# Kernel optimization log

Measured on AMD Instinct MI355X. Metric: run time of the kernel, lower is better.

## Reference

```python
import jax, jax.numpy as jnp
import numpy as np

N, E, H, HEADS, L, B = 16000, 256000, 192, 4, 4, 8
C = H // HEADS
VN, VE, T = 32, 8, 1000


def _sin_emb(t, dim):
    half = dim // 2
    freqs = jnp.exp(-np.log(10000.0) * jnp.arange(half, dtype=jnp.float32) / half)
    ang = t.astype(jnp.float32)[:, None] * freqs[None, :]
    return jnp.concatenate([jnp.sin(ang), jnp.cos(ang)], axis=-1)


def _ln(x, g, b, eps=1e-5):
    mu = jnp.mean(x, -1, keepdims=True)
    var = jnp.mean(jnp.square(x - mu), -1, keepdims=True)
    return (x - mu) * jax.lax.rsqrt(var + eps) * g + b


def setup_inputs():
    key = jax.random.key(0)
    ks = iter(jax.random.split(key, 64))
    p = lambda shape, s=0.02: jax.random.normal(next(ks), shape, jnp.float32) * s
    inp = {}
    inp['node_emb'] = p((VN, H))
    inp['edge_emb'] = p((VE, H))
    inp['time_w1'] = p((H, H)); inp['time_b1'] = jnp.zeros((H,), jnp.float32)
    inp['time_w2'] = p((H, H)); inp['time_b2'] = jnp.zeros((H,), jnp.float32)
    inp['mask_emb'] = p((2, H))
    inp['wq'] = p((L, H, H)); inp['bq'] = jnp.zeros((L, H), jnp.float32)
    inp['wk'] = p((L, H, H)); inp['bk'] = jnp.zeros((L, H), jnp.float32)
    inp['wv'] = p((L, H, H)); inp['bv'] = jnp.zeros((L, H), jnp.float32)
    inp['we'] = p((L, H, H))
    inp['wskip'] = p((L, H, H)); inp['bskip'] = jnp.zeros((L, H), jnp.float32)
    inp['wbeta'] = p((L, 3 * H))
    inp['ln_g'] = jnp.ones((L, H), jnp.float32); inp['ln_b'] = jnp.zeros((L, H), jnp.float32)
    inp['node_out_w'] = p((H, VN)); inp['node_out_b'] = jnp.zeros((VN,), jnp.float32)
    inp['edge_w1'] = p((4 * H, H)); inp['edge_b1'] = jnp.zeros((H,), jnp.float32)
    inp['edge_w2'] = p((H, VE)); inp['edge_b2'] = jnp.zeros((VE,), jnp.float32)
    inp['node_type'] = jax.random.randint(next(ks), (N,), 0, VN)
    inp['edge_type'] = jax.random.randint(next(ks), (E,), 0, VE)
    inp['edge_index'] = jax.random.randint(next(ks), (2, E), 0, N)
    inp['edit_mask'] = jax.random.randint(next(ks), (N,), 0, 2, dtype=jnp.int32)
    inp['node_batch'] = jnp.sort(jax.random.randint(next(ks), (N,), 0, B))
    inp['t_graph'] = jax.random.randint(next(ks), (B,), 1, T)
    return inp


def reference(node_emb, edge_emb, time_w1, time_b1, time_w2, time_b2, mask_emb,
              wq, bq, wk, bk, wv, bv, we, wskip, bskip, wbeta, ln_g, ln_b,
              node_out_w, node_out_b, edge_w1, edge_b1, edge_w2, edge_b2,
              node_type, edge_type, edge_index, edit_mask, node_batch, t_graph):
    src, dst = edge_index[0], edge_index[1]
    # time embedding: sinusoidal -> Linear -> SiLU -> Linear  => [B, H]
    t_vec = jax.nn.silu(_sin_emb(t_graph, H) @ time_w1 + time_b1) @ time_w2 + time_b2
    t_node = t_vec[node_batch]              # [N, H]
    t_edge = t_vec[node_batch[src]]         # [E, H]
    x = node_emb[node_type] + t_node + mask_emb[edit_mask]
    edge_attr = edge_emb[edge_type] + t_edge
    scale = 1.0 / np.sqrt(C)
    for l in range(L):
        q = (x @ wq[l] + bq[l]).reshape(N, HEADS, C)
        k = (x @ wk[l] + bk[l]).reshape(N, HEADS, C)
        v = (x @ wv[l] + bv[l]).reshape(N, HEADS, C)
        e = (edge_attr @ we[l]).reshape(E, HEADS, C)
        kj = k[src] + e                                   # [E, heads, C]
        score = jnp.sum(q[dst] * kj, axis=-1) * scale      # [E, heads]
        m = jax.ops.segment_max(score, dst, num_segments=N)
        ex = jnp.exp(score - m[dst])
        denom = jax.ops.segment_sum(ex, dst, num_segments=N)
        alpha = ex / denom[dst]
        msg = (v[src] + e) * alpha[..., None]              # [E, heads, C]
        out = jax.ops.segment_sum(msg, dst, num_segments=N).reshape(N, H)
        xr = x @ wskip[l] + bskip[l]
        beta = jax.nn.sigmoid(jnp.concatenate([out, xr, out - xr], -1) @ wbeta[l])[:, None]
        h = beta * xr + (1.0 - beta) * out
        x = _ln(x + h, ln_g[l], ln_b[l])
    node_logits = x @ node_out_w + node_out_b
    edge_feat = jnp.concatenate([x[src], x[dst], edge_attr, t_edge], -1)  # [E, 4H]
    edge_logits = jax.nn.silu(edge_feat @ edge_w1 + edge_b1) @ edge_w2 + edge_b2
    return node_logits, edge_logits
```

## Files before the change

kernel.cpp:

```cpp
#include <hip/hip_runtime.h>
#include <hip/hip_bf16.h>
#include <math.h>

#define NN 16000
#define NPAD 16128
#define NE 256000
#define H 192
#define RP 256
#define KVR 512
#define NL 4
#define NBATCH 8
#define VEt 8
#define HH (H*H)
#define EML 16

typedef __hip_bfloat16 bf16;
typedef unsigned short u16;
typedef unsigned char u8;
typedef unsigned int u32;
typedef __attribute__((ext_vector_type(8))) short bfrag_t;
typedef __attribute__((ext_vector_type(4))) float facc_t;
typedef __attribute__((ext_vector_type(4))) float f4;
typedef __attribute__((ext_vector_type(2))) unsigned int u32x2;
typedef __attribute__((ext_vector_type(2))) float f2v;

__device__ __forceinline__ bf16 f2b(float v){ return __float2bfloat16(v); }
__device__ __forceinline__ int rfl(int v){ return __builtin_amdgcn_readfirstlane(v); }

__device__ __forceinline__ unsigned enc8sw(float x){
    unsigned u = __float_as_uint(x);
    unsigned s = (u >> 24) & 0x80u;
    float ax = fabsf(x);
    if(ax >= 448.f) return s | 0x7Eu;
    if(ax < 0.015625f){
        int q = (int)rintf(ax * 512.f);
        return s | (unsigned)q;
    }
    unsigned au = u & 0x7FFFFFFFu;
    unsigned lsb = (au >> 20) & 1u;
    au += 0x7FFFFu + lsb;
    unsigned E = (au >> 23) - 127u;
    unsigned M = (au >> 20) & 7u;
    if((int)E > 8) return s | 0x7Eu;
    return s | ((E + 7u) << 3) | M;
}
__device__ __forceinline__ unsigned enc8(float x){
#if __has_builtin(__builtin_amdgcn_cvt_pk_fp8_f32)
    return (u32)__builtin_amdgcn_cvt_pk_fp8_f32(x, x, 0, false) & 0xFFu;
#else
    return enc8sw(x);
#endif
}
template<int SEL>
__device__ __forceinline__ float dec8s(u32 w){
#if __has_builtin(__builtin_amdgcn_cvt_f32_fp8)
    return __builtin_amdgcn_cvt_f32_fp8((int)w, SEL);
#else
    unsigned v = (w >> (SEL*8)) & 0xFFu;
    unsigned e = (v >> 3) & 15u, m = v & 7u;
    float mag = e ? __builtin_ldexpf((float)(8u + m), (int)e - 10)
                  : __builtin_ldexpf((float)m, -9);
    return (v & 0x80u) ? -mag : mag;
#endif
}
__device__ __forceinline__ f2v dec8pk01(u32 w){
#if __has_builtin(__builtin_amdgcn_cvt_pk_f32_fp8)
    return __builtin_amdgcn_cvt_pk_f32_fp8((int)w, false);
#else
    f2v r; r.x = dec8s<0>(w); r.y = dec8s<1>(w); return r;
#endif
}
__device__ __forceinline__ float frcp(float x){
#if __has_builtin(__builtin_amdgcn_rcpf)
    return __builtin_amdgcn_rcpf(x);
#else
    return 1.f/x;
#endif
}

__global__ void k_sentinel(float* __restrict__ out, float v){ out[0] = v; }

__global__ void k_prep0(const float* __restrict__ wq, const float* __restrict__ wk,
                        const float* __restrict__ wv, const float* __restrict__ wsk,
                        const float* __restrict__ w1, const float* __restrict__ now,
                        const float* __restrict__ ew2, u16* __restrict__ wt,
                        const int* __restrict__ tg, const float* __restrict__ tw1,
                        const float* __restrict__ tb1, const float* __restrict__ tw2,
                        const float* __restrict__ tb2, float* __restrict__ tvec,
                        int* __restrict__ cnt){
    int blk = blockIdx.x;
    if(blk < 160){
        int mat = blk >> 3, ys = blk & 7;
        if(mat < 18){
            const float* src;
            if(mat < 4)       src = wq  + (size_t)mat*HH;
            else if(mat < 8)  src = wk  + (size_t)(mat-4)*HH;
            else if(mat < 12) src = wv  + (size_t)(mat-8)*HH;
            else if(mat < 16) src = wsk + (size_t)(mat-12)*HH;
            else              src = w1  + (size_t)(mat-16)*HH;
            u16* dst = wt + (size_t)mat*HH;
            const int slice = HH/8;
            int base = ys*slice;
            for(int i = base + threadIdx.x; i < base + slice; i += blockDim.x){
                int k = i / H, n = i % H;
                bf16 b = f2b(src[i]);
                dst[n*H + k] = *(u16*)&b;
            }
        } else if(mat == 18){
            u16* dst = wt + (size_t)18*HH;
            const int slice = (32*192)/8;
            int base = ys*slice;
            for(int i = base + threadIdx.x; i < base + slice; i += blockDim.x){
                int k = i >> 5, n = i & 31;
                bf16 b = f2b(now[i]);
                dst[n*192 + k] = *(u16*)&b;
            }
        } else {
            u16* dst = wt + (size_t)18*HH + 32*192;
            const int slice = (16*192)/8;
            int base = ys*slice;
            for(int i = base + threadIdx.x; i < base + slice; i += blockDim.x){
                int k = i >> 4, n = i & 15;
                float v = (n < 8) ? ew2[k*8 + n] : 0.f;
                bf16 b = f2b(v);
                dst[n*192 + k] = *(u16*)&b;
            }
        }
    } else if(blk < 168){
        int b = blk - 160, j = threadIdx.x;
        __shared__ float emb[H], h1[H];
        float t = (float)tg[b];
        if(j < 96){
            float fr = __expf(-logf(10000.0f) * (float)j / 96.0f);
            float ang = t * fr;
            emb[j]      = sinf(ang);
            emb[j + 96] = cosf(ang);
        }
        __syncthreads();
        if(j < H){
            float acc = tb1[j];
            for(int k = 0; k < H; k++) acc += emb[k] * tw1[k*H + j];
            h1[j] = acc / (1.f + __expf(-acc));
        }
        __syncthreads();
        if(j < H){
            float acc2 = tb2[j];
            for(int k = 0; k < H; k++) acc2 += h1[k] * tw2[k*H + j];
            tvec[b*H + j] = acc2;
        }
    } else {
        int i = (blk - 168)*256 + threadIdx.x;
        if(i < NN+1) cnt[i] = 0;
    }
}

__global__ void k_prep1(const float* __restrict__ nemb, const float* __restrict__ memb,
                        const float* __restrict__ tvec, const int* __restrict__ ntype,
                        const int* __restrict__ emask, const int* __restrict__ nbatch,
                        float* __restrict__ x, u16* __restrict__ xb,
                        const int* __restrict__ edst, int* __restrict__ cnt,
                        const float* __restrict__ eemb, const float* __restrict__ we,
                        const float* __restrict__ w1, const float* __restrict__ b1,
                        u16* __restrict__ etab, u16* __restrict__ ctab){
    int blk = blockIdx.x;
    if(blk < 3000){
        int idx4 = (blk*256 + threadIdx.x)*4;
        int n = idx4 / H, c = idx4 % H;
        f4 nv = *(const f4*)(nemb + (size_t)ntype[n]*H + c);
        f4 tv = *(const f4*)(tvec + (size_t)nbatch[n]*H + c);
        f4 mv = *(const f4*)(memb + (size_t)emask[n]*H + c);
        f4 v; v.x = nv.x+tv.x+mv.x; v.y = nv.y+tv.y+mv.y;
              v.z = nv.z+tv.z+mv.z; v.w = nv.w+tv.w+mv.w;
        *(f4*)(x + idx4) = v;
        bf16 b0 = f2b(v.x), b1v = f2b(v.y), b2 = f2b(v.z), b3 = f2b(v.w);
        u16* xbp = xb + idx4;
        xbp[0] = *(u16*)&b0; xbp[1] = *(u16*)&b1v; xbp[2] = *(u16*)&b2; xbp[3] = *(u16*)&b3;
    } else if(blk < 4000){
        int e = (blk - 3000)*256 + threadIdx.x;
        atomicAdd(&cnt[edst[e]], 1);
    } else {
        int blk2 = blk - 4000;
        int c = threadIdx.x;
        __shared__ float a[H];
        if(blk2 < NL*64){
            int l = blk2 >> 6, idx = blk2 & 63, b = idx >> 3, et = idx & 7;
            if(c < H) a[c] = eemb[et*H + c] + tvec[b*H + c];
            __syncthreads();
            if(c < H){
                float acc = 0.f;
                const float* w = we + (size_t)l*HH;
                for(int k = 0; k < H; k++) acc += a[k] * w[k*H + c];
                bf16 bv = f2b(acc);
                etab[(size_t)blk2*256 + (c/3)*4 + (c%3)] = *(u16*)&bv;
            }
        } else {
            int idx = blk2 - NL*64, b = idx >> 3, et = idx & 7;
            if(c < H) a[c] = eemb[et*H + c] + tvec[b*H + c];
            __syncthreads();
            if(c < H){
                float acc = b1[c];
                for(int k = 0; k < H; k++){
                    acc += a[k]          * w1[(size_t)(2*H + k)*H + c];
                    acc += tvec[b*H + k] * w1[(size_t)(3*H + k)*H + c];
                }
                bf16 bv = f2b(acc);
                ctab[(size_t)idx*256 + (c/3)*4 + (c%3)] = *(u16*)&bv;
            }
        }
    }
}

__global__ __launch_bounds__(1024) void k_scan(const int* __restrict__ cnt,
                                               int* __restrict__ ofs, int* __restrict__ cur){
    __shared__ int wsum[16];
    __shared__ int carry_s;
    int tid = threadIdx.x, lane = tid & 63, w = tid >> 6;
    if(tid == 0) carry_s = 0;
    __syncthreads();
    for(int base = 0; base < NN; base += 1024){
        int idx = base + tid;
        int v = (idx < NN) ? cnt[idx] : 0;
        int sc = v;
        #pragma unroll
        for(int o = 1; o < 64; o <<= 1){
            int t = __shfl_up(sc, o);
            if(lane >= o) sc += t;
        }
        if(lane == 63) wsum[w] = sc;
        __syncthreads();
        if(w == 0){
            int ws = (lane < 16) ? wsum[lane] : 0;
            #pragma unroll
            for(int o = 1; o < 16; o <<= 1){
                int t = __shfl_up(ws, o);
                if(lane >= o) ws += t;
            }
            if(lane < 16) wsum[lane] = ws;
        }
        __syncthreads();
        int wbase = (w > 0) ? wsum[w-1] : 0;
        int c = carry_s;
        int excl = c + wbase + sc - v;
        if(idx < NN){ ofs[idx] = excl; cur[idx] = excl; }
        __syncthreads();
        if(tid == 0) carry_s = c + wsum[15];
        __syncthreads();
    }
    if(threadIdx.x == 0) ofs[NN] = carry_s;
}
__global__ void k_scatter(const int* __restrict__ esrc, const int* __restrict__ edst,
                          const int* __restrict__ etype, const int* __restrict__ nbatch,
                          int* __restrict__ cur, int2* __restrict__ spair, int4* __restrict__ eprep){
    int e = blockIdx.x*blockDim.x + threadIdx.x;
    if(e >= NE) return;
    int s = esrc[e], d = edst[e];
    int ct = (nbatch[s]*VEt + etype[e])*KVR;
    int pos = atomicAdd(&cur[d], 1);
    int2 se; se.x = s*KVR; se.y = ct;
    spair[pos] = se;
    eprep[e] = make_int4(s*RP, d*RP, ct, 0);
}

struct GemmP {
    const u16* wt[4];
    const float* bias[4];
    void* out[4];
    int obf[4];
};
__global__ __launch_bounds__(256) void k_gemm(const u16* __restrict__ A, GemmP P){
    int oi = blockIdx.y / 3, nt = blockIdx.y % 3;
    const u16* Wt = P.wt[oi];
    const float* bias = P.bias[oi];
    int wave = rfl(threadIdx.x >> 6), lane = threadIdx.x & 63;
    int quad = lane >> 4, l16 = lane & 15;
    int m0 = blockIdx.x*256 + wave*64;
    int n0 = nt*64;
    facc_t acc[4][4];
    #pragma unroll
    for(int i = 0; i < 4; i++)
        #pragma unroll
        for(int j = 0; j < 4; j++){ acc[i][j][0]=0.f; acc[i][j][1]=0.f; acc[i][j][2]=0.f; acc[i][j][3]=0.f; }
    #pragma unroll
    for(int kc = 0; kc < 6; kc++){
        int kb = kc*32 + quad*8;
        bfrag_t af[4], bg[4];
        #pragma unroll
        for(int i = 0; i < 4; i++) af[i] = *(const bfrag_t*)(A  + (size_t)(m0 + i*16 + l16)*H + kb);
        #pragma unroll
        for(int j = 0; j < 4; j++) bg[j] = *(const bfrag_t*)(Wt + (size_t)(n0 + j*16 + l16)*H + kb);
        #pragma unroll
        for(int i = 0; i < 4; i++)
            #pragma unroll
            for(int j = 0; j < 4; j++)
                acc[i][j] = __builtin_amdgcn_mfma_f32_16x16x32_bf16(af[i], bg[j], acc[i][j], 0, 0, 0);
    }
    float bv[4];
    #pragma unroll
    for(int j = 0; j < 4; j++) bv[j] = bias ? bias[n0 + j*16 + l16] : 0.f;
    int mode = P.obf[oi];
    if(mode == 5){
        u16* outp = (u16*)P.out[oi];
        int hoff[4];
        #pragma unroll
        for(int j = 0; j < 4; j++){
            int c = n0 + j*16 + l16;
            hoff[j] = (c/3)*4 + (c%3);
        }
        #pragma unroll
        for(int i = 0; i < 4; i++){
            int rb = m0 + i*16 + quad*4;
            #pragma unroll
            for(int r = 0; r < 4; r++){
                int row = rb + r;
                if(row < NN){
                    #pragma unroll
                    for(int j = 0; j < 4; j++){
                        bf16 b = f2b(acc[i][j][r] + bv[j]);
                        outp[(size_t)row*256 + hoff[j]] = *(u16*)&b;
                    }
                }
            }
        }
    } else if(mode != 0){
        u8* out = (u8*)P.out[oi];
        int rstride = (mode == 2) ? RP : KVR;
        int mult    = (mode == 2) ? 4  : 8;
        int koff    = (mode == 4) ? 4  : 0;
        int byteoff[4];
        #pragma unroll
        for(int j = 0; j < 4; j++){
            int c = n0 + j*16 + l16;
            byteoff[j] = (c/3)*mult + (c%3) + koff;
        }
        #pragma unroll
        for(int i = 0; i < 4; i++){
            int rb = m0 + i*16 + quad*4;
            #pragma unroll
            for(int r = 0; r < 4; r++){
                int row = rb + r;
                if(row < NN){
                    #pragma unroll
                    for(int j = 0; j < 4; j++)
                        out[(size_t)row*rstride + byteoff[j]] = (u8)enc8(acc[i][j][r] + bv[j]);
                }
            }
        }
    } else {
        float* out = (float*)P.out[oi];
        #pragma unroll
        for(int i = 0; i < 4; i++){
            int rb = m0 + i*16 + quad*4;
            #pragma unroll
            for(int r = 0; r < 4; r++){
                int row = rb + r;
                if(row < NN){
                    #pragma unroll
                    for(int j = 0; j < 4; j++)
                        out[(size_t)row*H + n0 + j*16 + l16] = acc[i][j][r] + bv[j];
                }
            }
        }
    }
}

__global__ __launch_bounds__(256) void k_attn(
    const u8* __restrict__ Qb, const u8* __restrict__ KVb,
    const u8* __restrict__ XRp,
    const u16* __restrict__ etab, const int* __restrict__ ofs,
    const int2* __restrict__ spair,
    const float* __restrict__ wb, const float* __restrict__ lng, const float* __restrict__ lnb,
    float* __restrict__ x, u16* __restrict__ xb)
{
    int wv = rfl(threadIdx.x >> 6);
    int n = blockIdx.x*4 + wv;
    int lane = threadIdx.x & 63;
    int lane8 = lane*8;
    int ch = lane*3;
    size_t base = (size_t)n*H + ch;
    const float scale = 0.14433756729740646f;
    u32x2 qw = *(const u32x2*)(Qb + (size_t)n*512 + lane8);
    float q0 = __uint_as_float(qw.x << 16);
    float q1 = __uint_as_float(qw.x & 0xffff0000u);
    float q2 = __uint_as_float(qw.y << 16);
    int p0 = ofs[n], p1 = ofs[n+1];
    float lac[4]  = {0.f,0.f,0.f,0.f};
    float ac0[4]  = {0.f,0.f,0.f,0.f};
    float ac1[4]  = {0.f,0.f,0.f,0.f};
    float ac2[4]  = {0.f,0.f,0.f,0.f};
    const u8* etb = (const u8*)etab;
    int p = p0;
    u32x2 kvc[4], ewc[4];
    bool have = (p + 3 < p1);
    if(have){
        #pragma unroll
        for(int t = 0; t < 4; t++){
            int2 se = spair[p+t];
            kvc[t] = *(const u32x2*)(KVb + se.x + lane8);
            ewc[t] = *(const u32x2*)(etb + se.y + lane8);
        }
    }
    while(have){
        int pn = p + 4;
        bool more = (pn + 3 < p1);
        u32x2 kvn[4], ewn[4];
        if(more){
            #pragma unroll
            for(int t = 0; t < 4; t++){
                int2 se = spair[pn+t];
                kvn[t] = *(const u32x2*)(KVb + se.x + lane8);
                ewn[t] = *(const u32x2*)(etb + se.y + lane8);
            }
        }
        float e0[4], e1[4], e2[4], tt[4];
        #pragma unroll
        for(int t = 0; t < 4; t++){
            e0[t] = __uint_as_float(ewc[t].x << 16);
            e1[t] = __uint_as_float(ewc[t].x & 0xffff0000u);
            e2[t] = __uint_as_float(ewc[t].y << 16);
            f2v k01 = dec8pk01(kvc[t].x);
            float k2 = dec8s<2>(kvc[t].x);
            tt[t] = q0*(k01.x+e0[t]) + q1*(k01.y+e1[t]) + q2*(k2+e2[t]);
        }
        #pragma unroll
        for(int o = 1; o <= 8; o <<= 1){
            #pragma unroll
            for(int t = 0; t < 4; t++) tt[t] += __shfl_xor(tt[t], o);
        }
        #pragma unroll
        for(int t = 0; t < 4; t++){
            float sc = fminf(fmaxf(tt[t]*scale, -60.f), 60.f);
            float pw = __expf(sc);
            f2v v01 = dec8pk01(kvc[t].y);
            float v2 = dec8s<2>(kvc[t].y);
            lac[t] += pw;
            ac0[t] += pw*(v01.x+e0[t]);
            ac1[t] += pw*(v01.y+e1[t]);
            ac2[t] += pw*(v2+e2[t]);
        }
        if(more){
            #pragma unroll
            for(int t = 0; t < 4; t++){ kvc[t] = kvn[t]; ewc[t] = ewn[t]; }
        }
        p = pn;
        have = more;
    }
    for(; p < p1; p++){
        int soA = spair[p].x, eoA = spair[p].y;
        u32x2 kvA = *(const u32x2*)(KVb + soA + lane8);
        u32x2 ewA = *(const u32x2*)(etb + eoA + lane8);
        float e0A = __uint_as_float(ewA.x << 16);
        float e1A = __uint_as_float(ewA.x & 0xffff0000u);
        float e2A = __uint_as_float(ewA.y << 16);
        f2v k01 = dec8pk01(kvA.x);
        float k2 = dec8s<2>(kvA.x);
        float tA = q0*(k01.x+e0A) + q1*(k01.y+e1A) + q2*(k2+e2A);
        tA += __shfl_xor(tA,1); tA += __shfl_xor(tA,2); tA += __shfl_xor(tA,4); tA += __shfl_xor(tA,8);
        float sc = fminf(fmaxf(tA*scale, -60.f), 60.f);
        float pw = __expf(sc);
        f2v v01 = dec8pk01(kvA.y);
        float v2 = dec8s<2>(kvA.y);
        lac[0] += pw;
        ac0[0] += pw*(v01.x+e0A);
        ac1[0] += pw*(v01.y+e1A);
        ac2[0] += pw*(v2+e2A);
    }
    float l  = (lac[0]+lac[1]) + (lac[2]+lac[3]);
    float a0 = (ac0[0]+ac0[1]) + (ac0[2]+ac0[3]);
    float a1 = (ac1[0]+ac1[1]) + (ac1[2]+ac1[3]);
    float a2 = (ac2[0]+ac2[1]) + (ac2[2]+ac2[3]);
    float inv = (p1 > p0) ? 1.f/l : 0.f;
    float o0 = a0*inv, o1 = a1*inv, o2 = a2*inv;
    u32x2 xrw = *(const u32x2*)(XRp + (size_t)n*512 + lane8);
    float xr0 = __uint_as_float(xrw.x << 16);
    float xr1 = __uint_as_float(xrw.x & 0xffff0000u);
    float xr2 = __uint_as_float(xrw.y << 16);
    float sd = o0*wb[ch]  + o1*wb[ch+1]  + o2*wb[ch+2]
             + xr0*wb[H+ch] + xr1*wb[H+ch+1] + xr2*wb[H+ch+2]
             + (o0-xr0)*wb[2*H+ch] + (o1-xr1)*wb[2*H+ch+1] + (o2-xr2)*wb[2*H+ch+2];
    sd += __shfl_xor(sd,1); sd += __shfl_xor(sd,2); sd += __shfl_xor(sd,4);
    sd += __shfl_xor(sd,8); sd += __shfl_xor(sd,16); sd += __shfl_xor(sd,32);
    float beta = 1.f/(1.f + __expf(-sd));
    float h0 = beta*xr0 + (1.f-beta)*o0;
    float h1 = beta*xr1 + (1.f-beta)*o1;
    float h2 = beta*xr2 + (1.f-beta)*o2;
    float y0 = x[base] + h0, y1 = x[base+1] + h1, y2 = x[base+2] + h2;
    float s3 = y0 + y1 + y2;
    float q3 = y0*y0 + y1*y1 + y2*y2;
    #pragma unroll
    for(int o = 1; o <= 32; o <<= 1){
        s3 += __shfl_xor(s3, o);
        q3 += __shfl_xor(q3, o);
    }
    float mean = s3 * (1.f/H);
    float var = fmaxf(q3*(1.f/H) - mean*mean, 0.f);
    float rs = rsqrtf(var + 1e-5f);
    float d0 = y0-mean, d1 = y1-mean, d2 = y2-mean;
    float z0 = d0*rs*lng[ch]   + lnb[ch];
    float z1 = d1*rs*lng[ch+1] + lnb[ch+1];
    float z2 = d2*rs*lng[ch+2] + lnb[ch+2];
    x[base] = z0; x[base+1] = z1; x[base+2] = z2;
    bf16 t0 = f2b(z0), t1 = f2b(z1), t2 = f2b(z2);
    xb[base] = *(u16*)&t0; xb[base+1] = *(u16*)&t1; xb[base+2] = *(u16*)&t2;
}

__global__ __launch_bounds__(256) void k_nodeout(const u16* __restrict__ A, const u16* __restrict__ Wt,
                                                 const float* __restrict__ b, float* __restrict__ out){
    int wave = rfl(threadIdx.x >> 6), lane = threadIdx.x & 63;
    int quad = lane >> 4, l16 = lane & 15;
    int m0 = blockIdx.x*256 + wave*64;
    facc_t acc[4][2];
    #pragma unroll
    for(int i = 0; i < 4; i++)
        #pragma unroll
        for(int j = 0; j < 2; j++){ acc[i][j][0]=0.f; acc[i][j][1]=0.f; acc[i][j][2]=0.f; acc[i][j][3]=0.f; }
    #pragma unroll
    for(int kc = 0; kc < 6; kc++){
        int kb = kc*32 + quad*8;
        bfrag_t af[4], bg[2];
        #pragma unroll
        for(int i = 0; i < 4; i++) af[i] = *(const bfrag_t*)(A  + (size_t)(m0 + i*16 + l16)*H + kb);
        #pragma unroll
        for(int j = 0; j < 2; j++) bg[j] = *(const bfrag_t*)(Wt + (size_t)(j*16 + l16)*H + kb);
        #pragma unroll
        for(int i = 0; i < 4; i++)
            #pragma unroll
            for(int j = 0; j < 2; j++)
                acc[i][j] = __builtin_amdgcn_mfma_f32_16x16x32_bf16(af[i], bg[j], acc[i][j], 0, 0, 0);
    }
    float bv[2];
    #pragma unroll
    for(int j = 0; j < 2; j++) bv[j] = b[j*16 + l16];
    #pragma unroll
    for(int i = 0; i < 4; i++){
        int rb = m0 + i*16 + quad*4;
        #pragma unroll
        for(int r = 0; r < 4; r++){
            int row = rb + r;
            if(row < NN){
                #pragma unroll
                for(int j = 0; j < 2; j++)
                    out[(size_t)row*32 + j*16 + l16] = acc[i][j][r] + bv[j];
            }
        }
    }
}

__global__ __launch_bounds__(256) void k_edgemlp(
    const int4* __restrict__ eprep,
    const u8* __restrict__ xs1, const u8* __restrict__ xd1, const u16* __restrict__ ctab,
    const u16* __restrict__ w2t, const float* __restrict__ b2p, float* __restrict__ out)
{
    __shared__ u16 hbuf[4][16][200];
    int wave = rfl(threadIdx.x >> 6);
    int lane = threadIdx.x & 63;
    int lane8 = lane*8;
    int l16 = lane & 15, quad = lane >> 4;
    int wid = blockIdx.x*4 + wave;
    int e0 = wid*EML;
    const u8* ctb = (const u8*)ctab;
    bfrag_t bg[6];
    #pragma unroll
    for(int kc = 0; kc < 6; kc++)
        bg[kc] = *(const bfrag_t*)(w2t + (size_t)l16*192 + kc*32 + quad*8);
    for(int eb = 0; eb < EML; eb += 2){
        int4 epX = eprep[e0 + eb];
        int4 epY = eprep[e0 + eb + 1];
        u32 awX = *(const u32*)(xs1 + epX.x + lane*4);
        u32 awY = *(const u32*)(xs1 + epY.x + lane*4);
        u32 bwX = *(const u32*)(xd1 + epX.y + lane*4);
        u32 bwY = *(const u32*)(xd1 + epY.y + lane*4);
        u32x2 cwX = *(const u32x2*)(ctb + epX.z + lane8);
        u32x2 cwY = *(const u32x2*)(ctb + epY.z + lane8);
        float cfX0 = __uint_as_float(cwX.x << 16);
        float cfX1 = __uint_as_float(cwX.x & 0xffff0000u);
        float cfX2 = __uint_as_float(cwX.y << 16);
        float cfY0 = __uint_as_float(cwY.x << 16);
        float cfY1 = __uint_as_float(cwY.x & 0xffff0000u);
        float cfY2 = __uint_as_float(cwY.y << 16);
        f2v aX = dec8pk01(awX), bX = dec8pk01(bwX);
        f2v aY = dec8pk01(awY), bY = dec8pk01(bwY);
        float aX2 = dec8s<2>(awX), bX2 = dec8s<2>(bwX);
        float aY2 = dec8s<2>(awY), bY2 = dec8s<2>(bwY);
        float hX0, hX1, hX2, hY0, hY1, hY2;
        { float v = aX.x+bX.x+cfX0; hX0 = v*frcp(1.f+__expf(-v)); }
        { float v = aX.y+bX.y+cfX1; hX1 = v*frcp(1.f+__expf(-v)); }
        { float v = aX2 +bX2 +cfX2; hX2 = v*frcp(1.f+__expf(-v)); }
        { float v = aY.x+bY.x+cfY0; hY0 = v*frcp(1.f+__expf(-v)); }
        { float v = aY.y+bY.y+cfY1; hY1 = v*frcp(1.f+__expf(-v)); }
        { float v = aY2 +bY2 +cfY2; hY2 = v*frcp(1.f+__expf(-v)); }
        u16* rowX = &hbuf[wave][eb][0];
        u16* rowY = &hbuf[wave][eb+1][0];
        bf16 x0 = f2b(hX0), x1 = f2b(hX1), x2 = f2b(hX2);
        bf16 y0 = f2b(hY0), y1 = f2b(hY1), y2 = f2b(hY2);
        rowX[lane*3+0] = *(u16*)&x0; rowX[lane*3+1] = *(u16*)&x1; rowX[lane*3+2] = *(u16*)&x2;
        rowY[lane*3+0] = *(u16*)&y0; rowY[lane*3+1] = *(u16*)&y1; rowY[lane*3+2] = *(u16*)&y2;
    }
    __syncthreads();
    facc_t acc;
    acc[0]=0.f; acc[1]=0.f; acc[2]=0.f; acc[3]=0.f;
    #pragma unroll
    for(int kc = 0; kc < 6; kc++){
        bfrag_t af = *(const bfrag_t*)&hbuf[wave][l16][kc*32 + quad*8];
        acc = __builtin_amdgcn_mfma_f32_16x16x32_bf16(af, bg[kc], acc, 0, 0, 0);
    }
    if(l16 < 8){
        float bo = b2p[l16];
        #pragma unroll
        for(int r = 0; r < 4; r++){
            int e = e0 + quad*4 + r;
            out[(size_t)e*8 + l16] = acc[r] + bo;
        }
    }
}

extern "C" void kernel_launch(void* const* d_in, const int* in_sizes, int n_in,
                              void* d_out, int out_size, void* d_ws, size_t ws_size,
                              hipStream_t stream)
{
    {
        int bad = -1;
        if(n_in != 31) bad = 100;
        else {
            const int chk_idx[9] = {0, 7, 16, 21, 23, 26, 27, 29, 30};
            const int chk_sz [9] = {32*H, NL*HH, NL*3*H, 4*HH, H*8, NE, 2*NE, NN, NBATCH};
            for(int i = 0; i < 9; i++) if(in_sizes[chk_idx[i]] != chk_sz[i]){ bad = chk_idx[i]; break; }
        }
        if(bad >= 0){ k_sentinel<<<1,1,0,stream>>>((float*)d_out, 20000.f + 256.f*bad); return; }
        if(out_size != NN*32 + NE*8){ k_sentinel<<<1,1,0,stream>>>((float*)d_out, 30000.f); return; }
    }

    const float* node_emb = (const float*)d_in[0];
    const float* edge_emb = (const float*)d_in[1];
    const float* time_w1  = (const float*)d_in[2];
    const float* time_b1  = (const float*)d_in[3];
    const float* time_w2  = (const float*)d_in[4];
    const float* time_b2  = (const float*)d_in[5];
    const float* mask_emb = (const float*)d_in[6];
    const float* wq       = (const float*)d_in[7];
    const float* bq       = (const float*)d_in[8];
    const float* wk       = (const float*)d_in[9];
    const float* bk       = (const float*)d_in[10];
    const float* wv       = (const float*)d_in[11];
    const float* bv       = (const float*)d_in[12];
    const float* we       = (const float*)d_in[13];
    const float* wskip    = (const float*)d_in[14];
    const float* bskip    = (const float*)d_in[15];
    const float* wbeta    = (const float*)d_in[16];
    const float* ln_g     = (const float*)d_in[17];
    const float* ln_b     = (const float*)d_in[18];
    const float* now      = (const float*)d_in[19];
    const float* nob      = (const float*)d_in[20];
    const float* ew1      = (const float*)d_in[21];
    const float* eb1      = (const float*)d_in[22];
    const float* ew2      = (const float*)d_in[23];
    const float* eb2      = (const float*)d_in[24];
    const int* node_type  = (const int*)d_in[25];
    const int* edge_type  = (const int*)d_in[26];
    const int* edge_index = (const int*)d_in[27];
    const int* edit_mask  = (const int*)d_in[28];
    const int* node_batch = (const int*)d_in[29];
    const int* t_graph    = (const int*)d_in[30];
    const int* esrc = edge_index;
    const int* edst = edge_index + NE;

    char* wsb = (char*)d_ws;
    size_t off = 0;
    auto take = [&](size_t bytes) -> char* {
        char* r = wsb + off;
        off += (bytes + 255) & ~(size_t)255;
        return r;
    };
    float* tvec = (float*)take((size_t)NBATCH*H*4);
    float* x    = (float*)take((size_t)NN*H*4);
    u16*   xb   = (u16*)  take((size_t)NPAD*H*2);
    u8*    Qb   = (u8*)   take((size_t)NN*512);
    u8*    KVb  = (u8*)   take((size_t)NN*KVR);
    u8*    XRp  = (u8*)   take((size_t)NN*512);
    u8*    xs1  = (u8*)   take((size_t)NN*RP);
    u8*    xd1  = (u8*)   take((size_t)NN*RP);
    u16*   etab = (u16*)  take((size_t)NL*64*KVR);
    u16*   ctab = (u16*)  take((size_t)64*KVR);
    u16*   wt   = (u16*)  take((size_t)(18*HH + 32*192 + 16*192)*2);
    int* cnt    = (int*)  take((size_t)(NN+1)*4);
    int* offa   = (int*)  take((size_t)(NN+1)*4);
    int* cur    = (int*)  take((size_t)(NN+1)*4);
    int2* spair = (int2*) take((size_t)NE*8);
    int4* eprep = (int4*) take((size_t)NE*16);

    if(ws_size < off){
        k_sentinel<<<1,1,0,stream>>>((float*)d_out, 10000.f + (float)(ws_size >> 20));
        return;
    }

    u16* w32t = wt + (size_t)18*HH;
    u16* w2t  = w32t + 32*192;

    k_prep0<<<231, 256, 0, stream>>>(wq, wk, wv, wskip, ew1, now, ew2, wt,
                                     t_graph, time_w1, time_b1, time_w2, time_b2, tvec, cnt);
    k_prep1<<<4320, 256, 0, stream>>>(node_emb, mask_emb, tvec, node_type, edit_mask, node_batch,
                                      x, xb, edst, cnt, edge_emb, we, ew1, eb1, etab, ctab);
    k_scan<<<1, 1024, 0, stream>>>(cnt, offa, cur);
    k_scatter<<<NE/256, 256, 0, stream>>>(esrc, edst, edge_type, node_batch, cur, spair, eprep);

    for(int l = 0; l < NL; l++){
        GemmP P;
        P.wt[0] = wt + (size_t)(0  + l)*HH;  P.bias[0] = bq   + (size_t)l*H;  P.out[0] = Qb;  P.obf[0] = 5;
        P.wt[1] = wt + (size_t)(4  + l)*HH;  P.bias[1] = bk   + (size_t)l*H;  P.out[1] = KVb; P.obf[1] = 3;
        P.wt[2] = wt + (size_t)(8  + l)*HH;  P.bias[2] = bv   + (size_t)l*H;  P.out[2] = KVb; P.obf[2] = 4;
        P.wt[3] = wt + (size_t)(12 + l)*HH;  P.bias[3] = bskip+ (size_t)l*H;  P.out[3] = XRp; P.obf[3] = 5;
        k_gemm<<<dim3(63, 12), 256, 0, stream>>>(xb, P);
        k_attn<<<NN/4, 256, 0, stream>>>(Qb, KVb, XRp, etab + (size_t)l*64*256, offa, spair,
                                         wbeta + (size_t)l*3*H, ln_g + (size_t)l*H,
                                         ln_b + (size_t)l*H, x, xb);
    }
    {
        GemmP P;
        P.wt[0] = wt + (size_t)16*HH; P.bias[0] = nullptr; P.out[0] = xs1; P.obf[0] = 2;
        P.wt[1] = wt + (size_t)17*HH; P.bias[1] = nullptr; P.out[1] = xd1; P.obf[1] = 2;
        P.wt[2] = P.wt[0]; P.bias[2] = nullptr; P.out[2] = xs1; P.obf[2] = 2;
        P.wt[3] = P.wt[0]; P.bias[3] = nullptr; P.out[3] = xs1; P.obf[3] = 2;
        k_gemm<<<dim3(63, 6), 256, 0, stream>>>(xb, P);
    }
    k_nodeout<<<63, 256, 0, stream>>>(xb, w32t, nob, (float*)d_out);
    k_edgemlp<<<NE/(4*EML), 256, 0, stream>>>(eprep, xs1, xd1, ctab,
                                              w2t, eb2, (float*)d_out + (size_t)NN*32);
}
```

Measured before the change: 460.9 us.

## Remap GEMM output columns so each lane owns a channel triple for packed stores

Result: no change. 469.0 us (+1.8%).

```diff
diff --git a/kernel.cpp b/kernel.cpp
--- a/kernel.cpp
+++ b/kernel.cpp
@@ -49,6 +49,15 @@
     return (u32)__builtin_amdgcn_cvt_pk_fp8_f32(x, x, 0, false) & 0xFFu;
 #else
     return enc8sw(x);
+#endif
+}
+__device__ __forceinline__ u32 enc3(float f0, float f1, float f2){
+#if __has_builtin(__builtin_amdgcn_cvt_pk_fp8_f32)
+    u32 w = (u32)__builtin_amdgcn_cvt_pk_fp8_f32(f0, f1, 0, false);
+    w = (u32)__builtin_amdgcn_cvt_pk_fp8_f32(f2, f2, (int)w, true);
+    return w;
+#else
+    return enc8sw(f0) | (enc8sw(f1) << 8) | (enc8sw(f2) << 16);
 #endif
 }
 template<int SEL>
@@ -268,96 +277,58 @@
     int obf[4];
 };
 __global__ __launch_bounds__(256) void k_gemm(const u16* __restrict__ A, GemmP P){
-    int oi = blockIdx.y / 3, nt = blockIdx.y % 3;
+    int oi = blockIdx.y >> 2, nt = blockIdx.y & 3;
     const u16* Wt = P.wt[oi];
     const float* bias = P.bias[oi];
     int wave = rfl(threadIdx.x >> 6), lane = threadIdx.x & 63;
     int quad = lane >> 4, l16 = lane & 15;
     int m0 = blockIdx.x*256 + wave*64;
-    int n0 = nt*64;
-    facc_t acc[4][4];
+    int nrow = nt*48 + l16*3;
+    int g = nt*16 + l16;
+    facc_t acc[4][3];
     #pragma unroll
     for(int i = 0; i < 4; i++)
         #pragma unroll
-        for(int j = 0; j < 4; j++){ acc[i][j][0]=0.f; acc[i][j][1]=0.f; acc[i][j][2]=0.f; acc[i][j][3]=0.f; }
+        for(int j = 0; j < 3; j++){ acc[i][j][0]=0.f; acc[i][j][1]=0.f; acc[i][j][2]=0.f; acc[i][j][3]=0.f; }
     #pragma unroll
     for(int kc = 0; kc < 6; kc++){
         int kb = kc*32 + quad*8;
-        bfrag_t af[4], bg[4];
+        bfrag_t af[4], bg[3];
         #pragma unroll
         for(int i = 0; i < 4; i++) af[i] = *(const bfrag_t*)(A  + (size_t)(m0 + i*16 + l16)*H + kb);
         #pragma unroll
-        for(int j = 0; j < 4; j++) bg[j] = *(const bfrag_t*)(Wt + (size_t)(n0 + j*16 + l16)*H + kb);
+        for(int j = 0; j < 3; j++) bg[j] = *(const bfrag_t*)(Wt + (size_t)(nrow + j)*H + kb);
         #pragma unroll
         for(int i = 0; i < 4; i++)
             #pragma unroll
-            for(int j = 0; j < 4; j++)
+            for(int j = 0; j < 3; j++)
                 acc[i][j] = __builtin_amdgcn_mfma_f32_16x16x32_bf16(af[i], bg[j], acc[i][j], 0, 0, 0);
     }
-    float bv[4];
-    #pragma unroll
-    for(int j = 0; j < 4; j++) bv[j] = bias ? bias[n0 + j*16 + l16] : 0.f;
+    float bv0 = bias ? bias[nrow]     : 0.f;
+    float bv1 = bias ? bias[nrow + 1] : 0.f;
+    float bv2 = bias ? bias[nrow + 2] : 0.f;
     int mode = P.obf[oi];
-    if(mode == 5){
-        u16* outp = (u16*)P.out[oi];
-        int hoff[4];
-        #pragma unroll
-        for(int j = 0; j < 4; j++){
-            int c = n0 + j*16 + l16;
-            hoff[j] = (c/3)*4 + (c%3);
-        }
-        #pragma unroll
-        for(int i = 0; i < 4; i++){
-            int rb = m0 + i*16 + quad*4;
-            #pragma unroll
-            for(int r = 0; r < 4; r++){
-                int row = rb + r;
-                if(row < NN){
-                    #pragma unroll
-                    for(int j = 0; j < 4; j++){
-                        bf16 b = f2b(acc[i][j][r] + bv[j]);
-                        outp[(size_t)row*256 + hoff[j]] = *(u16*)&b;
-                    }
-                }
-            }
-        }
-    } else if(mode != 0){
-        u8* out = (u8*)P.out[oi];
-        int rstride = (mode == 2) ? RP : KVR;
-        int mult    = (mode == 2) ? 4  : 8;
-        int koff    = (mode == 4) ? 4  : 0;
-        int byteoff[4];
-        #pragma unroll
-        for(int j = 0; j < 4; j++){
-            int c = n0 + j*16 + l16;
-            byteoff[j] = (c/3)*mult + (c%3) + koff;
-        }
-        #pragma unroll
-        for(int i = 0; i < 4; i++){
-            int rb = m0 + i*16 + quad*4;
-            #pragma unroll
-            for(int r = 0; r < 4; r++){
-                int row = rb + r;
-                if(row < NN){
-                    #pragma unroll
-                    for(int j = 0; j < 4; j++)
-                        out[(size_t)row*rstride + byteoff[j]] = (u8)enc8(acc[i][j][r] + bv[j]);
-                }
-            }
-        }
-    } else {
-        float* out = (float*)P.out[oi];
-        #pragma unroll
-        for(int i = 0; i < 4; i++){
-            int rb = m0 + i*16 + quad*4;
-            #pragma unroll
-            for(int r = 0; r < 4; r++){
-                int row = rb + r;
-                if(row < NN){
-                    #pragma unroll
-                    for(int j = 0; j < 4; j++)
-                        out[(size_t)row*H + n0 + j*16 + l16] = acc[i][j][r] + bv[j];
-                }
+    #pragma unroll
+    for(int i = 0; i < 4; i++){
+        int rb = m0 + i*16 + quad*4;
+        #pragma unroll
+        for(int r = 0; r < 4; r++){
+            int row = rb + r;
+            if(row >= NN) continue;
+            float f0 = acc[i][0][r] + bv0;
+            float f1 = acc[i][1][r] + bv1;
+            float f2 = acc[i][2][r] + bv2;
+            if(mode == 5){
+                bf16 h0 = f2b(f0), h1 = f2b(f1), h2 = f2b(f2);
+                u32x2 d;
+                d.x = (u32)*(u16*)&h0 | ((u32)*(u16*)&h1 << 16);
+                d.y = (u32)*(u16*)&h2;
+                *(u32x2*)((u8*)P.out[oi] + (size_t)row*512 + g*8) = d;
+            } else if(mode == 2){
+                *(u32*)((u8*)P.out[oi] + (size_t)row*256 + g*4) = enc3(f0, f1, f2);
+            } else {
+                int koff = (mode == 4) ? 4 : 0;
+                *(u32*)((u8*)P.out[oi] + (size_t)row*512 + g*8 + koff) = enc3(f0, f1, f2);
             }
         }
     }
@@ -708,7 +679,7 @@
         P.wt[1] = wt + (size_t)(4  + l)*HH;  P.bias[1] = bk   + (size_t)l*H;  P.out[1] = KVb; P.obf[1] = 3;
         P.wt[2] = wt + (size_t)(8  + l)*HH;  P.bias[2] = bv   + (size_t)l*H;  P.out[2] = KVb; P.obf[2] = 4;
         P.wt[3] = wt + (size_t)(12 + l)*HH;  P.bias[3] = bskip+ (size_t)l*H;  P.out[3] = XRp; P.obf[3] = 5;
-        k_gemm<<<dim3(63, 12), 256, 0, stream>>>(xb, P);
+        k_gemm<<<dim3(63, 16), 256, 0, stream>>>(xb, P);
         k_attn<<<NN/4, 256, 0, stream>>>(Qb, KVb, XRp, etab + (size_t)l*64*256, offa, spair,
                                          wbeta + (size_t)l*3*H, ln_g + (size_t)l*H,
                                          ln_b + (size_t)l*H, x, xb);
@@ -719,7 +690,7 @@
         P.wt[1] = wt + (size_t)17*HH; P.bias[1] = nullptr; P.out[1] = xd1; P.obf[1] = 2;
         P.wt[2] = P.wt[0]; P.bias[2] = nullptr; P.out[2] = xs1; P.obf[2] = 2;
         P.wt[3] = P.wt[0]; P.bias[3] = nullptr; P.out[3] = xs1; P.obf[3] = 2;
-        k_gemm<<<dim3(63, 6), 256, 0, stream>>>(xb, P);
+        k_gemm<<<dim3(63, 8), 256, 0, stream>>>(xb, P);
     }
     k_nodeout<<<63, 256, 0, stream>>>(xb, w32t, nob, (float*)d_out);
     k_edgemlp<<<NE/(4*EML), 256, 0, stream>>>(eprep, xs1, xd1, ctab,
```
